# Kernel tuning notes

Measured on AMD Instinct MI355X. Metric: run time of the kernel, lower is better.

## Reference

```python
import jax, jax.numpy as jnp
import numpy as np

SCALE = 0.125  # softmax_scale = 1/sqrt(head_dim=64)


def setup_inputs() -> dict:
    key = jax.random.key(0)
    ks = jax.random.split(key, 5)
    B, H, S, D = 1, 8, 256, 64
    shp = (B, H, S, D)
    return {
        "q": jax.random.normal(ks[0], shp, dtype=jnp.float32),
        "k1": jax.random.normal(ks[1], shp, dtype=jnp.float32),
        "k2": jax.random.normal(ks[2], shp, dtype=jnp.float32),
        "v1": jax.random.normal(ks[3], shp, dtype=jnp.float32),
        "v2": jax.random.normal(ks[4], shp, dtype=jnp.float32),
    }


def reference(q, k1, k2, v1, v2):
    # Trittention: 3-way score over all (i, j) key pairs per query q.
    # s[b,h,q,i,j] = sum_d Q[q,d] * K1[i,d] * K2[j,d]  (scaled)
    B, H, S, D = q.shape
    s = jnp.einsum("bhqd,bhid,bhjd->bhqij", q, k1, k2) * SCALE  # [B,H,S,S,S]
    s_flat = s.reshape(B, H, S, S * S).astype(jnp.float32)
    m = jax.nn.logsumexp(s_flat, axis=-1)               # [B,H,S] flash-style stats
    p = jax.nn.softmax(s_flat, axis=-1).reshape(B, H, S, S, S)
    # O = sum_{i,j} P * (V1_i + V2_j)
    o = (jnp.einsum("bhqij,bhid->bhqd", p, v1)
         + jnp.einsum("bhqij,bhjd->bhqd", p, v2)).astype(q.dtype)
    return o, m
```

## Files before the change

kernel.cpp:

```cpp
#include <hip/hip_runtime.h>
#include <hip/hip_bf16.h>

typedef __attribute__((ext_vector_type(8))) short short8;
typedef __attribute__((ext_vector_type(4))) float f32x4;

static constexpr int S_ = 256;
static constexpr int D_ = 64;
static constexpr float QSCALE = 0.125f * 1.44269504088896340736f;

__device__ __forceinline__ unsigned cvt_pk_bf16(float lo, float hi) {
    unsigned r;
    asm("v_cvt_pk_bf16_f32 %0, %1, %2" : "=v"(r) : "v"(lo), "v"(hi));
    return r;
}

__global__ __launch_bounds__(256, 2) void tritt_fused(
    const float* __restrict__ qg, const float* __restrict__ k1g,
    const float* __restrict__ k2g, const float* __restrict__ v1g,
    const float* __restrict__ v2g, float* __restrict__ outg)
{
    __shared__ unsigned short sK2[S_ * D_];
    __shared__ float sPi[2][S_];
    __shared__ float sPjH[4][S_];

    const int tid = threadIdx.x;
    const int qt = blockIdx.x & 127;
    const int h  = blockIdx.x >> 7;
    const int q0 = qt * 2;

    const float* K1h = k1g + h * (S_ * D_);
    const float* K2h = k2g + h * (S_ * D_);

    #pragma unroll
    for (int it = 0; it < 16; ++it) {
        const int e4  = tid * 4 + it * 1024;
        const int row = e4 >> 6, d = e4 & 63;
        const int idx = row * 64 + (d ^ ((row & 7) << 3));
        const float4 b = *(const float4*)(K2h + e4);
        uint2 pb; pb.x = cvt_pk_bf16(b.x, b.y); pb.y = cvt_pk_bf16(b.z, b.w);
        *(uint2*)&sK2[idx] = pb;
    }

    const int w     = tid >> 6;
    const int l     = tid & 63;
    const int g     = l >> 4;
    const int sub   = l & 15;
    const int q     = w & 1;
    const int ihalf = w >> 1;
    const int ibase0 = ihalf * 128;

    float qs[2][8];
    {
        const float* Qrow = qg + (h * S_ + q0 + q) * D_;
        #pragma unroll
        for (int k = 0; k < 2; ++k) {
            const f32x4 a = *(const f32x4*)(Qrow + k * 32 + g * 8);
            const f32x4 b = *(const f32x4*)(Qrow + k * 32 + g * 8 + 4);
            qs[k][0]=a[0]*QSCALE; qs[k][1]=a[1]*QSCALE; qs[k][2]=a[2]*QSCALE; qs[k][3]=a[3]*QSCALE;
            qs[k][4]=b[0]*QSCALE; qs[k][5]=b[1]*QSCALE; qs[k][6]=b[2]*QSCALE; qs[k][7]=b[3]*QSCALE;
        }
    }
    __syncthreads();

    float pjreg[16];
    #pragma unroll
    for (int a = 0; a < 16; ++a) pjreg[a] = 0.f;

    for (int pass = 0; pass < 4; ++pass) {
        short8 af[2][2];
        #pragma unroll
        for (int t = 0; t < 2; ++t) {
            const int arow = ibase0 + pass * 32 + t * 16 + sub;
            #pragma unroll
            for (int k = 0; k < 2; ++k) {
                const f32x4 a = *(const f32x4*)(K1h + arow * 64 + k * 32 + g * 8);
                const f32x4 b = *(const f32x4*)(K1h + arow * 64 + k * 32 + g * 8 + 4);
                union { unsigned u[4]; short8 s; } pk;
                pk.u[0] = cvt_pk_bf16(a[0] * qs[k][0], a[1] * qs[k][1]);
                pk.u[1] = cvt_pk_bf16(a[2] * qs[k][2], a[3] * qs[k][3]);
                pk.u[2] = cvt_pk_bf16(b[0] * qs[k][4], b[1] * qs[k][5]);
                pk.u[3] = cvt_pk_bf16(b[2] * qs[k][6], b[3] * qs[k][7]);
                af[t][k] = pk.s;
            }
        }

        float pireg[2][4];
        #pragma unroll
        for (int t = 0; t < 2; ++t)
            #pragma unroll
            for (int r = 0; r < 4; ++r) pireg[t][r] = 0.f;

        #pragma unroll
        for (int jc = 0; jc < 4; ++jc) {
            #pragma unroll
            for (int jt = 0; jt < 4; ++jt) {
                const int jrow = jc * 64 + jt * 16 + sub;
                const int jsw  = (jrow & 7) << 3;
                const short8 b0 = *(const short8*)&sK2[jrow * 64 + ((g * 8) ^ jsw)];
                const short8 b1 = *(const short8*)&sK2[jrow * 64 + ((32 + g * 8) ^ jsw)];
                f32x4 acc0 = __builtin_amdgcn_mfma_f32_16x16x32_bf16(af[0][0], b0, (f32x4){0.f,0.f,0.f,0.f}, 0, 0, 0);
                f32x4 acc1 = __builtin_amdgcn_mfma_f32_16x16x32_bf16(af[1][0], b0, (f32x4){0.f,0.f,0.f,0.f}, 0, 0, 0);
                acc0 = __builtin_amdgcn_mfma_f32_16x16x32_bf16(af[0][1], b1, acc0, 0, 0, 0);
                acc1 = __builtin_amdgcn_mfma_f32_16x16x32_bf16(af[1][1], b1, acc1, 0, 0, 0);
                float e0[4], e1[4];
                #pragma unroll
                for (int r = 0; r < 4; ++r) {
                    e0[r] = __builtin_amdgcn_exp2f(acc0[r]);
                    e1[r] = __builtin_amdgcn_exp2f(acc1[r]);
                    pireg[0][r] += e0[r];
                    pireg[1][r] += e1[r];
                }
                const float s0 = (e0[0] + e0[1]) + (e0[2] + e0[3]);
                const float s1 = (e1[0] + e1[1]) + (e1[2] + e1[3]);
                pjreg[jc * 4 + jt] += s0 + s1;
            }
        }

        #pragma unroll
        for (int t = 0; t < 2; ++t)
            #pragma unroll
            for (int r = 0; r < 4; ++r) {
                float v = pireg[t][r];
                v += __shfl_xor(v, 1); v += __shfl_xor(v, 2);
                v += __shfl_xor(v, 4); v += __shfl_xor(v, 8);
                if (sub == 0) sPi[q][ibase0 + pass * 32 + t * 16 + g * 4 + r] = v;
            }
    }

    #pragma unroll
    for (int jj = 0; jj < 16; ++jj) {
        float v = pjreg[jj];
        v += __shfl_xor(v, 16); v += __shfl_xor(v, 32);
        if (l < 16) sPjH[w][jj * 16 + l] = v;
    }
    __syncthreads();

    float* sTmp = (float*)sK2;
    {
        const int d = l;
        const float* V1h = v1g + h * (S_ * D_);
        const float* V2h = v2g + h * (S_ * D_);
        float p0 = 0.f, p1 = 0.f;
        #pragma unroll 4
        for (int rb = 0; rb < 16; ++rb) {
            const int r0 = w * 64 + rb * 4;
            const f32x4 pi0 = *(const f32x4*)&sPi[0][r0];
            const f32x4 pi1 = *(const f32x4*)&sPi[1][r0];
            const f32x4 pa0 = *(const f32x4*)&sPjH[0][r0];
            const f32x4 pa1 = *(const f32x4*)&sPjH[1][r0];
            const f32x4 pa2 = *(const f32x4*)&sPjH[2][r0];
            const f32x4 pa3 = *(const f32x4*)&sPjH[3][r0];
            #pragma unroll
            for (int e = 0; e < 4; ++e) {
                const float v1 = V1h[(r0 + e) * D_ + d];
                const float v2 = V2h[(r0 + e) * D_ + d];
                p0 += pi0[e] * v1 + (pa0[e] + pa2[e]) * v2;
                p1 += pi1[e] * v1 + (pa1[e] + pa3[e]) * v2;
            }
        }
        sTmp[w * 128 + 0 * 64 + d] = p0;
        sTmp[w * 128 + 1 * 64 + d] = p1;
    }
    __syncthreads();
    if (tid < 128) {
        const int qq = tid >> 6, d = tid & 63;
        const float oo = sTmp[0 * 128 + qq * 64 + d] + sTmp[1 * 128 + qq * 64 + d]
                       + sTmp[2 * 128 + qq * 64 + d] + sTmp[3 * 128 + qq * 64 + d];
        float ls = sPi[qq][d] + sPi[qq][64 + d] + sPi[qq][128 + d] + sPi[qq][192 + d];
        ls += __shfl_xor(ls, 1);  ls += __shfl_xor(ls, 2);  ls += __shfl_xor(ls, 4);
        ls += __shfl_xor(ls, 8);  ls += __shfl_xor(ls, 16); ls += __shfl_xor(ls, 32);
        outg[(h * S_ + q0 + qq) * D_ + d] = oo / ls;
        if (d == 0)
            outg[8 * S_ * D_ + h * S_ + q0 + qq] = logf(ls);
    }
}

extern "C" void kernel_launch(void* const* d_in, const int* in_sizes, int n_in,
                              void* d_out, int out_size, void* d_ws, size_t ws_size,
                              hipStream_t stream) {
    const float* q  = (const float*)d_in[0];
    const float* k1 = (const float*)d_in[1];
    const float* k2 = (const float*)d_in[2];
    const float* v1 = (const float*)d_in[3];
    const float* v2 = (const float*)d_in[4];
    float* out = (float*)d_out;
    tritt_fused<<<dim3(8 * (S_ / 2)), dim3(256), 0, stream>>>(q, k1, k2, v1, v2, out);
}
```

Before: 49.22 us.

## Process both queries per wave to reuse each K2 LDS fragment across twice the MFMAs

Each wave now handles both queries of the block over a 64-row slice of K1, rather than one query over a 128-row slice. Every K2 fragment read from LDS therefore feeds eight MFMAs instead of four, halving LDS traffic per MFMA and giving more independent MFMA chains to hide latency. This doubles the accumulator registers (pjreg, pireg, acc) and adds an extra LDS reduction step plus barrier to merge the per-wave pj partial sums. The extra register pressure could lower occupancy under the launch bound of two blocks.

```diff
diff --git a/kernel.cpp b/kernel.cpp
--- a/kernel.cpp
+++ b/kernel.cpp
@@ -21,7 +21,7 @@
 {
     __shared__ unsigned short sK2[S_ * D_];
     __shared__ float sPi[2][S_];
-    __shared__ float sPjH[4][S_];
+    __shared__ float sPjH[4][2][S_];
 
     const int tid = threadIdx.x;
     const int qt = blockIdx.x & 127;
@@ -41,97 +41,134 @@
         *(uint2*)&sK2[idx] = pb;
     }
 
-    const int w     = tid >> 6;
-    const int l     = tid & 63;
-    const int g     = l >> 4;
-    const int sub   = l & 15;
-    const int q     = w & 1;
-    const int ihalf = w >> 1;
-    const int ibase0 = ihalf * 128;
-
-    float qs[2][8];
-    {
+    const int w   = tid >> 6;
+    const int l   = tid & 63;
+    const int g   = l >> 4;
+    const int sub = l & 15;
+    const int cb0 = (g * 8) ^ ((sub & 7) << 3);
+    const int cb1 = (32 + g * 8) ^ ((sub & 7) << 3);
+    const int jb  = sub * 64;
+
+    float qs[2][2][8];
+    #pragma unroll
+    for (int q = 0; q < 2; ++q) {
         const float* Qrow = qg + (h * S_ + q0 + q) * D_;
         #pragma unroll
         for (int k = 0; k < 2; ++k) {
             const f32x4 a = *(const f32x4*)(Qrow + k * 32 + g * 8);
             const f32x4 b = *(const f32x4*)(Qrow + k * 32 + g * 8 + 4);
-            qs[k][0]=a[0]*QSCALE; qs[k][1]=a[1]*QSCALE; qs[k][2]=a[2]*QSCALE; qs[k][3]=a[3]*QSCALE;
-            qs[k][4]=b[0]*QSCALE; qs[k][5]=b[1]*QSCALE; qs[k][6]=b[2]*QSCALE; qs[k][7]=b[3]*QSCALE;
-        }
-    }
-    __syncthreads();
-
-    float pjreg[16];
-    #pragma unroll
-    for (int a = 0; a < 16; ++a) pjreg[a] = 0.f;
-
-    for (int pass = 0; pass < 4; ++pass) {
-        short8 af[2][2];
+            #pragma unroll
+            for (int e = 0; e < 4; ++e) {
+                qs[q][k][e]     = a[e] * QSCALE;
+                qs[q][k][4 + e] = b[e] * QSCALE;
+            }
+        }
+    }
+    __syncthreads();
+
+    float pjreg[2][16];
+    #pragma unroll
+    for (int q = 0; q < 2; ++q)
+        #pragma unroll
+        for (int a = 0; a < 16; ++a) pjreg[q][a] = 0.f;
+
+    for (int pass = 0; pass < 2; ++pass) {
+        short8 af[2][2][2];
         #pragma unroll
         for (int t = 0; t < 2; ++t) {
-            const int arow = ibase0 + pass * 32 + t * 16 + sub;
+            const int arow = w * 64 + pass * 32 + t * 16 + sub;
             #pragma unroll
             for (int k = 0; k < 2; ++k) {
                 const f32x4 a = *(const f32x4*)(K1h + arow * 64 + k * 32 + g * 8);
                 const f32x4 b = *(const f32x4*)(K1h + arow * 64 + k * 32 + g * 8 + 4);
-                union { unsigned u[4]; short8 s; } pk;
-                pk.u[0] = cvt_pk_bf16(a[0] * qs[k][0], a[1] * qs[k][1]);
-                pk.u[1] = cvt_pk_bf16(a[2] * qs[k][2], a[3] * qs[k][3]);
-                pk.u[2] = cvt_pk_bf16(b[0] * qs[k][4], b[1] * qs[k][5]);
-                pk.u[3] = cvt_pk_bf16(b[2] * qs[k][6], b[3] * qs[k][7]);
-                af[t][k] = pk.s;
-            }
-        }
-
-        float pireg[2][4];
+                #pragma unroll
+                for (int q = 0; q < 2; ++q) {
+                    union { unsigned u[4]; short8 s; } pk;
+                    pk.u[0] = cvt_pk_bf16(a[0] * qs[q][k][0], a[1] * qs[q][k][1]);
+                    pk.u[1] = cvt_pk_bf16(a[2] * qs[q][k][2], a[3] * qs[q][k][3]);
+                    pk.u[2] = cvt_pk_bf16(b[0] * qs[q][k][4], b[1] * qs[q][k][5]);
+                    pk.u[3] = cvt_pk_bf16(b[2] * qs[q][k][6], b[3] * qs[q][k][7]);
+                    af[t][q][k] = pk.s;
+                }
+            }
+        }
+
+        float pireg[2][2][4];
         #pragma unroll
         for (int t = 0; t < 2; ++t)
             #pragma unroll
-            for (int r = 0; r < 4; ++r) pireg[t][r] = 0.f;
+            for (int q = 0; q < 2; ++q)
+                #pragma unroll
+                for (int r = 0; r < 4; ++r) pireg[t][q][r] = 0.f;
 
         #pragma unroll
         for (int jc = 0; jc < 4; ++jc) {
             #pragma unroll
             for (int jt = 0; jt < 4; ++jt) {
-                const int jrow = jc * 64 + jt * 16 + sub;
-                const int jsw  = (jrow & 7) << 3;
-                const short8 b0 = *(const short8*)&sK2[jrow * 64 + ((g * 8) ^ jsw)];
-                const short8 b1 = *(const short8*)&sK2[jrow * 64 + ((32 + g * 8) ^ jsw)];
-                f32x4 acc0 = __builtin_amdgcn_mfma_f32_16x16x32_bf16(af[0][0], b0, (f32x4){0.f,0.f,0.f,0.f}, 0, 0, 0);
-                f32x4 acc1 = __builtin_amdgcn_mfma_f32_16x16x32_bf16(af[1][0], b0, (f32x4){0.f,0.f,0.f,0.f}, 0, 0, 0);
-                acc0 = __builtin_amdgcn_mfma_f32_16x16x32_bf16(af[0][1], b1, acc0, 0, 0, 0);
-                acc1 = __builtin_amdgcn_mfma_f32_16x16x32_bf16(af[1][1], b1, acc1, 0, 0, 0);
-                float e0[4], e1[4];
+                const int e0 = jb + jc * 4096 + jt * 1024;
+                const short8 b0 = *(const short8*)&sK2[e0 + cb0];
+                const short8 b1 = *(const short8*)&sK2[e0 + cb1];
+                f32x4 acc[2][2];
+                #pragma unroll
+                for (int t = 0; t < 2; ++t)
+                    #pragma unroll
+                    for (int q = 0; q < 2; ++q)
+                        acc[t][q] = __builtin_amdgcn_mfma_f32_16x16x32_bf16(af[t][q][0], b0, (f32x4){0.f,0.f,0.f,0.f}, 0, 0, 0);
+                #pragma unroll
+                for (int t = 0; t < 2; ++t)
+                    #pragma unroll
+                    for (int q = 0; q < 2; ++q)
+                        acc[t][q] = __builtin_amdgcn_mfma_f32_16x16x32_bf16(af[t][q][1], b1, acc[t][q], 0, 0, 0);
+                float e_[2][2][4];
+                #pragma unroll
+                for (int t = 0; t < 2; ++t)
+                    #pragma unroll
+                    for (int q = 0; q < 2; ++q)
+                        #pragma unroll
+                        for (int r = 0; r < 4; ++r) {
+                            e_[t][q][r] = __builtin_amdgcn_exp2f(acc[t][q][r]);
+                            pireg[t][q][r] += e_[t][q][r];
+                        }
+                #pragma unroll
+                for (int q = 0; q < 2; ++q) {
+                    const float s0 = (e_[0][q][0] + e_[0][q][1]) + (e_[0][q][2] + e_[0][q][3]);
+                    const float s1 = (e_[1][q][0] + e_[1][q][1]) + (e_[1][q][2] + e_[1][q][3]);
+                    pjreg[q][jc * 4 + jt] += s0 + s1;
+                }
+            }
+        }
+
+        #pragma unroll
+        for (int t = 0; t < 2; ++t)
+            #pragma unroll
+            for (int q = 0; q < 2; ++q)
                 #pragma unroll
                 for (int r = 0; r < 4; ++r) {
-                    e0[r] = __builtin_amdgcn_exp2f(acc0[r]);
-                    e1[r] = __builtin_amdgcn_exp2f(acc1[r]);
-                    pireg[0][r] += e0[r];
-                    pireg[1][r] += e1[r];
+                    float v = pireg[t][q][r];
+                    v += __shfl_xor(v, 1); v += __shfl_xor(v, 2);
+                    v += __shfl_xor(v, 4); v += __shfl_xor(v, 8);
+                    if (sub == 0) sPi[q][w * 64 + pass * 32 + t * 16 + g * 4 + r] = v;
                 }
-                const float s0 = (e0[0] + e0[1]) + (e0[2] + e0[3]);
-                const float s1 = (e1[0] + e1[1]) + (e1[2] + e1[3]);
-                pjreg[jc * 4 + jt] += s0 + s1;
-            }
-        }
-
-        #pragma unroll
-        for (int t = 0; t < 2; ++t)
-            #pragma unroll
-            for (int r = 0; r < 4; ++r) {
-                float v = pireg[t][r];
-                v += __shfl_xor(v, 1); v += __shfl_xor(v, 2);
-                v += __shfl_xor(v, 4); v += __shfl_xor(v, 8);
-                if (sub == 0) sPi[q][ibase0 + pass * 32 + t * 16 + g * 4 + r] = v;
-            }
-    }
-
-    #pragma unroll
-    for (int jj = 0; jj < 16; ++jj) {
-        float v = pjreg[jj];
-        v += __shfl_xor(v, 16); v += __shfl_xor(v, 32);
-        if (l < 16) sPjH[w][jj * 16 + l] = v;
+    }
+
+    #pragma unroll
+    for (int q = 0; q < 2; ++q)
+        #pragma unroll
+        for (int jj = 0; jj < 16; ++jj) {
+            float v = pjreg[q][jj];
+            v += __shfl_xor(v, 16); v += __shfl_xor(v, 32);
+            if (l < 16) sPjH[w][q][jj * 16 + l] = v;
+        }
+    __syncthreads();
+
+    if (tid < 128) {
+        const int q  = tid >> 6;
+        const int j4 = (tid & 63) * 4;
+        f32x4 s = *(const f32x4*)&sPjH[0][q][j4];
+        s += *(const f32x4*)&sPjH[1][q][j4];
+        s += *(const f32x4*)&sPjH[2][q][j4];
+        s += *(const f32x4*)&sPjH[3][q][j4];
+        *(f32x4*)&sPjH[0][q][j4] = s;
     }
     __syncthreads();
 
@@ -146,16 +183,14 @@
             const int r0 = w * 64 + rb * 4;
             const f32x4 pi0 = *(const f32x4*)&sPi[0][r0];
             const f32x4 pi1 = *(const f32x4*)&sPi[1][r0];
-            const f32x4 pa0 = *(const f32x4*)&sPjH[0][r0];
-            const f32x4 pa1 = *(const f32x4*)&sPjH[1][r0];
-            const f32x4 pa2 = *(const f32x4*)&sPjH[2][r0];
-            const f32x4 pa3 = *(const f32x4*)&sPjH[3][r0];
+            const f32x4 pj0 = *(const f32x4*)&sPjH[0][0][r0];
+            const f32x4 pj1 = *(const f32x4*)&sPjH[0][1][r0];
             #pragma unroll
             for (int e = 0; e < 4; ++e) {
                 const float v1 = V1h[(r0 + e) * D_ + d];
                 const float v2 = V2h[(r0 + e) * D_ + d];
-                p0 += pi0[e] * v1 + (pa0[e] + pa2[e]) * v2;
-                p1 += pi1[e] * v1 + (pa1[e] + pa3[e]) * v2;
+                p0 += pi0[e] * v1 + pj0[e] * v2;
+                p1 += pi1[e] * v1 + pj1[e] * v2;
             }
         }
         sTmp[w * 128 + 0 * 64 + d] = p0;
```

Result: slower. 131.4 us (+166.9%).
